# Kernel optimization log

Measured on AMD Instinct MI355X. Metric: run time of the kernel, lower is better.

Reference implementation:

```python
import jax, jax.numpy as jnp
import numpy as np

B, S, E, D, A = 32, 2048, 1024, 1024, 1024


def setup_inputs() -> dict:
    key = jax.random.key(0)
    k1, k2, k3, k4, k5, k6, k7, k8 = jax.random.split(key, 8)
    # Kaiming-uniform-ish init scales (values don't matter for correctness)
    def lin(kw, kb, fan_in, fan_out):
        bound = 1.0 / np.sqrt(fan_in)
        W = jax.random.uniform(kw, (fan_out, fan_in), minval=-bound, maxval=bound, dtype=jnp.float32)
        b = jax.random.uniform(kb, (fan_out,), minval=-bound, maxval=bound, dtype=jnp.float32)
        return W, b
    W_enc, b_enc = lin(k1, k2, E, A)
    W_dec, b_dec = lin(k3, k4, D, A)
    W_v, b_v = lin(k5, k6, A, 1)
    encoder_out = jax.random.normal(k7, (B, S, E), dtype=jnp.float32)
    decoder_hidden = jax.random.normal(k8, (B, D), dtype=jnp.float32)
    return {
        "encoder_out": encoder_out,
        "decoder_hidden": decoder_hidden,
        "W_enc": W_enc, "b_enc": b_enc,
        "W_dec": W_dec, "b_dec": b_dec,
        "W_v": W_v, "b_v": b_v,
    }


def reference(encoder_out, decoder_hidden, W_enc, b_enc, W_dec, b_dec, W_v, b_v):
    # encoder_proj: [B, S, A]
    encoder_proj = jnp.einsum('bse,ae->bsa', encoder_out, W_enc) + b_enc
    # decoder_proj: [B, 1, A]
    decoder_proj = (jnp.einsum('bd,ad->ba', decoder_hidden, W_dec) + b_dec)[:, None, :]
    # scores: [B, S] (V projects attention_dim -> 1)
    scores = jnp.einsum('bsa,a->bs', jnp.tanh(encoder_proj + decoder_proj), W_v[0]) + b_v[0]
    alpha = jax.nn.softmax(scores, axis=1)  # [B, S]
    context = jnp.einsum('bse,bs->be', encoder_out, alpha)  # [B, E]
    return (context, alpha)
```

## Files before the change

kernel.cpp:

```cpp
#include <hip/hip_runtime.h>

typedef unsigned short ushort_t;
typedef __attribute__((ext_vector_type(8))) short short8;
typedef __attribute__((ext_vector_type(4))) float f32x4;


__device__ __forceinline__ ushort_t f2bf(float f) {
    unsigned u = __builtin_bit_cast(unsigned, f);
    u += 0x7fffu + ((u >> 16) & 1u);
    return (ushort_t)(u >> 16);
}

__device__ __forceinline__ float bf2f(ushort_t h) {
    unsigned u = ((unsigned)h) << 16;
    return __builtin_bit_cast(float, u);
}

__device__ __forceinline__ float tanh_fast(float x) {
    float e = __expf(2.0f * x);
    float r = __builtin_amdgcn_rcpf(e + 1.0f);
    return __builtin_fmaf(-2.0f, r, 1.0f);
}

__device__ __forceinline__ void gld16(const ushort_t* g, ushort_t* lds) {
    __builtin_amdgcn_global_load_lds(
        (const __attribute__((address_space(1))) unsigned int*)g,
        (__attribute__((address_space(3))) unsigned int*)lds, 16, 0, 0);
}


__global__ __launch_bounds__(256) void k_front(const float* __restrict__ enc,
                                               const float* __restrict__ Wenc,
                                               const float* __restrict__ dh,
                                               const float* __restrict__ Wd,
                                               const float* __restrict__ bd,
                                               const float* __restrict__ be,
                                               ushort_t* __restrict__ encB,
                                               ushort_t* __restrict__ wencB,
                                               float* __restrict__ dproj,
                                               float4* __restrict__ scores4) {
    const int bx = blockIdx.x;
    const int t = threadIdx.x;
    if (bx < 8192) {
        int i = bx * 256 + t;
        for (; i < 17055744; i += 2097152) {
            if (i < 16777216) {
                float4 v = ((const float4*)enc)[i];
                ushort4 o;
                o.x = f2bf(v.x); o.y = f2bf(v.y); o.z = f2bf(v.z); o.w = f2bf(v.w);
                ((ushort4*)encB)[i] = o;
            } else if (i < 17039360) {
                int j = i - 16777216;
                float4 v = ((const float4*)Wenc)[j];
                ushort4 o;
                o.x = f2bf(v.x); o.y = f2bf(v.y); o.z = f2bf(v.z); o.w = f2bf(v.w);
                ((ushort4*)wencB)[j] = o;
            } else {
                scores4[i - 17039360] = (float4){0.f, 0.f, 0.f, 0.f};
            }
        }
    } else {
        int wid = (bx - 8192) * 4 + (t >> 6);
        int lane = t & 63;
        int a = wid & 1023, b = wid >> 10;
        const float4* x = (const float4*)(dh + (size_t)b * 1024);
        const float4* wrow = (const float4*)(Wd + (size_t)a * 1024);
        float s = 0.f;
#pragma unroll
        for (int it = 0; it < 4; ++it) {
            int c = it * 64 + lane;
            float4 xv = x[c], wv = wrow[c];
            s += xv.x * wv.x + xv.y * wv.y + xv.z * wv.z + xv.w * wv.w;
        }
#pragma unroll
        for (int o = 1; o < 64; o <<= 1) s += __shfl_xor(s, o, 64);
        if (lane == 0) dproj[b * 1024 + a] = s + bd[a] + be[a];
    }
}


__global__ __launch_bounds__(512, 2) void k_gemm_scores(const ushort_t* __restrict__ A,
                                                        const ushort_t* __restrict__ Bm,
                                                        const float* __restrict__ dproj,
                                                        const float* __restrict__ Wv,
                                                        float* __restrict__ scores) {
    __shared__ __align__(16) ushort_t At[2][256 * 64];
    __shared__ __align__(16) ushort_t Bt[2][256 * 64];

    const int tid = threadIdx.x;
    const int lane = tid & 63;
    const int w = tid >> 6;
    const int wm = w >> 2, wn = w & 3;

    const int blk = blockIdx.x;
    const int xcd = blk & 7;
    const int idx = blk >> 3;
    const int blkN = idx & 3;
    const int blkM = xcd + ((idx >> 2) << 3);
    const long long arow0 = (long long)blkM * 256;
    const int brow0 = blkN * 256;

    const int sr = lane >> 3;
    const int sgrp = lane & 7;
    const int c8s = sgrp ^ sr;

    const int q = lane >> 4;
    const int ml = lane & 15;

    const ushort_t* ga = A + (arow0 + w * 8 + sr) * 1024 + c8s * 8;
    const ushort_t* gb = Bm + (long long)(brow0 + w * 8 + sr) * 1024 + c8s * 8;

    f32x4 acc[8][4];
#pragma unroll
    for (int i = 0; i < 8; ++i)
#pragma unroll
        for (int jj = 0; jj < 4; ++jj) acc[i][jj] = (f32x4){0.f, 0.f, 0.f, 0.f};

#pragma unroll
    for (int j = 0; j < 4; ++j) gld16(ga + j * 65536, &At[0][w * 512 + j * 4096]);
#pragma unroll
    for (int j = 0; j < 4; ++j) gld16(gb + j * 65536, &Bt[0][w * 512 + j * 4096]);
    ga += 64; gb += 64;
    __builtin_amdgcn_s_waitcnt(0);
    __syncthreads();

    for (int t = 0; t < 16; ++t) {
        const int cur = t & 1;
        if (t < 15) {
            const int nxt = cur ^ 1;
#pragma unroll
            for (int j = 0; j < 4; ++j) gld16(ga + j * 65536, &At[nxt][w * 512 + j * 4096]);
#pragma unroll
            for (int j = 0; j < 4; ++j) gld16(gb + j * 65536, &Bt[nxt][w * 512 + j * 4096]);
            ga += 64; gb += 64;
        }
#pragma unroll
        for (int kk = 0; kk < 2; ++kk) {
            const int kb = kk * 4;
            const int slot = (kb + q) ^ (ml & 7);
            short8 af[8], bfr[4];
#pragma unroll
            for (int i = 0; i < 8; ++i) {
                int row = wm * 128 + i * 16 + ml;
                af[i] = *(const short8*)&At[cur][row * 64 + slot * 8];
            }
#pragma unroll
            for (int jj = 0; jj < 4; ++jj) {
                int col = wn * 64 + jj * 16 + ml;
                bfr[jj] = *(const short8*)&Bt[cur][col * 64 + slot * 8];
            }
            __builtin_amdgcn_s_setprio(1);
#pragma unroll
            for (int i = 0; i < 8; ++i)
#pragma unroll
                for (int jj = 0; jj < 4; ++jj)
                    acc[i][jj] = __builtin_amdgcn_mfma_f32_16x16x32_bf16(
                        af[i], bfr[jj], acc[i][jj], 0, 0, 0);
            __builtin_amdgcn_s_setprio(0);
        }
        __builtin_amdgcn_s_waitcnt(0);
        __syncthreads();
    }

    const int bb = blkM >> 3;
    float dp[4], wv[4];
#pragma unroll
    for (int jj = 0; jj < 4; ++jj) {
        int a = blkN * 256 + wn * 64 + jj * 16 + ml;
        dp[jj] = dproj[bb * 1024 + a];
        wv[jj] = Wv[a];
    }
#pragma unroll
    for (int i = 0; i < 8; ++i) {
        float rs[4] = {0.f, 0.f, 0.f, 0.f};
#pragma unroll
        for (int jj = 0; jj < 4; ++jj) {
            f32x4 v = acc[i][jj];
            rs[0] += wv[jj] * tanh_fast(v.x + dp[jj]);
            rs[1] += wv[jj] * tanh_fast(v.y + dp[jj]);
            rs[2] += wv[jj] * tanh_fast(v.z + dp[jj]);
            rs[3] += wv[jj] * tanh_fast(v.w + dp[jj]);
        }
#pragma unroll
        for (int r = 0; r < 4; ++r)
#pragma unroll
            for (int o = 1; o < 16; o <<= 1) rs[r] += __shfl_xor(rs[r], o, 64);
        if (ml == 0) {
            long long m0 = arow0 + wm * 128 + i * 16 + q * 4;
            atomicAdd(&scores[m0 + 0], rs[0]);
            atomicAdd(&scores[m0 + 1], rs[1]);
            atomicAdd(&scores[m0 + 2], rs[2]);
            atomicAdd(&scores[m0 + 3], rs[3]);
        }
    }
}


__global__ __launch_bounds__(512) void k_ctx(const ushort_t* __restrict__ encB,
                                             const float* __restrict__ scores,
                                             float* __restrict__ out) {
    const int b = blockIdx.x, ec = blockIdx.y;
    const int t = threadIdx.x;
    const int l = t & 31, g = t >> 5;
    const int lane = t & 63, wv = t >> 6;
    __shared__ float al[2048];
    __shared__ float red[8];
    __shared__ f32x4 part[16][33];

    float4 v = ((const float4*)scores)[b * 512 + t];
    float mx = fmaxf(fmaxf(v.x, v.y), fmaxf(v.z, v.w));
#pragma unroll
    for (int o = 1; o < 64; o <<= 1) mx = fmaxf(mx, __shfl_xor(mx, o, 64));
    if (lane == 0) red[wv] = mx;
    __syncthreads();
    mx = red[0];
#pragma unroll
    for (int j = 1; j < 8; ++j) mx = fmaxf(mx, red[j]);
    float e0 = __expf(v.x - mx), e1 = __expf(v.y - mx);
    float e2 = __expf(v.z - mx), e3 = __expf(v.w - mx);
    float s = e0 + e1 + e2 + e3;
#pragma unroll
    for (int o = 1; o < 64; o <<= 1) s += __shfl_xor(s, o, 64);
    __syncthreads();
    if (lane == 0) red[wv] = s;
    __syncthreads();
    s = 0.f;
#pragma unroll
    for (int j = 0; j < 8; ++j) s += red[j];
    float inv = 1.0f / s;
    float4 a4 = (float4){e0 * inv, e1 * inv, e2 * inv, e3 * inv};
    ((float4*)al)[t] = a4;
    if (ec == 0) ((float4*)(out + 32768 + (size_t)b * 2048))[t] = a4;
    __syncthreads();

    const ushort_t* ep = encB + ((size_t)b * 2048 + g) * 1024 + ec * 128 + l * 4;
    f32x4 acc = (f32x4){0.f, 0.f, 0.f, 0.f};
#pragma unroll 8
    for (int it = 0; it < 128; ++it) {
        ushort4 ev = *(const ushort4*)(ep + (size_t)it * 16384);
        float a = al[g + it * 16];
        acc.x += a * bf2f(ev.x);
        acc.y += a * bf2f(ev.y);
        acc.z += a * bf2f(ev.z);
        acc.w += a * bf2f(ev.w);
    }
    part[g][l] = acc;
    __syncthreads();
    if (t < 32) {
        f32x4 ss = part[0][t];
#pragma unroll
        for (int gg = 1; gg < 16; ++gg) {
            f32x4 pp = part[gg][t];
            ss.x += pp.x; ss.y += pp.y; ss.z += pp.z; ss.w += pp.w;
        }
        *(float4*)(out + (size_t)b * 1024 + ec * 128 + t * 4) =
            (float4){ss.x, ss.y, ss.z, ss.w};
    }
}


extern "C" void kernel_launch(void* const* d_in, const int* in_sizes, int n_in,
                              void* d_out, int out_size, void* d_ws, size_t ws_size,
                              hipStream_t stream) {
    const float* enc  = (const float*)d_in[0];
    const float* dh   = (const float*)d_in[1];
    const float* Wenc = (const float*)d_in[2];
    const float* benc = (const float*)d_in[3];
    const float* Wdec = (const float*)d_in[4];
    const float* bdec = (const float*)d_in[5];
    const float* Wv   = (const float*)d_in[6];
    float* out = (float*)d_out;

    char* ws = (char*)d_ws;
    ushort_t* encB  = (ushort_t*)ws;
    ushort_t* wencB = (ushort_t*)(ws + 134217728ull);
    float* dproj    = (float*)(ws + 134217728ull + 2097152ull);
    float* scores   = (float*)(ws + 134217728ull + 2097152ull + 131072ull);

    k_front<<<16384, 256, 0, stream>>>(enc, Wenc, dh, Wdec, bdec, benc,
                                       encB, wencB, dproj, (float4*)scores);
    k_gemm_scores<<<1024, 512, 0, stream>>>(encB, wencB, dproj, Wv, scores);
    k_ctx<<<dim3(32, 8), 512, 0, stream>>>(encB, scores, out);
}
```

Measured before the change: 574.1 us.

## Triple-buffer A tiles and use counted vmcnt waits in scores GEMM

The GEMM main loop moves from a double-buffered A/B pipeline with a full waitcnt(0) per step to a triple-buffered A and double-buffered B rotation. It uses explicit s_waitcnt vmcnt(N) so each iteration waits only for the tile it is about to consume, leaving later prefetches in flight. The intent is to hide more global-load latency behind MFMA work and stop draining the load queue every iteration. The cost is LDS use rising from 128KB to 160KB per block, which fills the CU's LDS. The hand-counted vmcnt values must exactly match the load issue order.

```diff
diff --git a/kernel.cpp b/kernel.cpp
--- a/kernel.cpp
+++ b/kernel.cpp
@@ -84,7 +84,7 @@
                                                         const float* __restrict__ dproj,
                                                         const float* __restrict__ Wv,
                                                         float* __restrict__ scores) {
-    __shared__ __align__(16) ushort_t At[2][256 * 64];
+    __shared__ __align__(16) ushort_t At[3][256 * 64];
     __shared__ __align__(16) ushort_t Bt[2][256 * 64];
 
     const int tid = threadIdx.x;
@@ -107,8 +107,8 @@
     const int q = lane >> 4;
     const int ml = lane & 15;
 
-    const ushort_t* ga = A + (arow0 + w * 8 + sr) * 1024 + c8s * 8;
-    const ushort_t* gb = Bm + (long long)(brow0 + w * 8 + sr) * 1024 + c8s * 8;
+    const ushort_t* gA = A + (arow0 + w * 8 + sr) * 1024 + c8s * 8;
+    const ushort_t* gB = Bm + (long long)(brow0 + w * 8 + sr) * 1024 + c8s * 8;
 
     f32x4 acc[8][4];
 #pragma unroll
@@ -116,24 +116,27 @@
 #pragma unroll
         for (int jj = 0; jj < 4; ++jj) acc[i][jj] = (f32x4){0.f, 0.f, 0.f, 0.f};
 
-#pragma unroll
-    for (int j = 0; j < 4; ++j) gld16(ga + j * 65536, &At[0][w * 512 + j * 4096]);
-#pragma unroll
-    for (int j = 0; j < 4; ++j) gld16(gb + j * 65536, &Bt[0][w * 512 + j * 4096]);
-    ga += 64; gb += 64;
-    __builtin_amdgcn_s_waitcnt(0);
-    __syncthreads();
+    ushort_t* a0 = At[0]; ushort_t* a1 = At[1]; ushort_t* a2 = At[2];
+    ushort_t* b0 = Bt[0]; ushort_t* b1 = Bt[1];
+
+    auto stage = [&](const ushort_t* src, ushort_t* dst) {
+#pragma unroll
+        for (int j = 0; j < 4; ++j) gld16(src + j * 65536, dst + w * 512 + j * 4096);
+    };
+
+    stage(gA, a0); gA += 64;
+    stage(gB, b0); gB += 64;
+    stage(gA, a1); gA += 64;
+    stage(gB, b1); gB += 64;
+    stage(gA, a2); gA += 64;
 
     for (int t = 0; t < 16; ++t) {
-        const int cur = t & 1;
-        if (t < 15) {
-            const int nxt = cur ^ 1;
-#pragma unroll
-            for (int j = 0; j < 4; ++j) gld16(ga + j * 65536, &At[nxt][w * 512 + j * 4096]);
-#pragma unroll
-            for (int j = 0; j < 4; ++j) gld16(gb + j * 65536, &Bt[nxt][w * 512 + j * 4096]);
-            ga += 64; gb += 64;
-        }
+        if (t < 14)       asm volatile("s_waitcnt vmcnt(12)" ::: "memory");
+        else if (t == 14) asm volatile("s_waitcnt vmcnt(8)"  ::: "memory");
+        else              asm volatile("s_waitcnt vmcnt(0)"  ::: "memory");
+        __builtin_amdgcn_s_barrier();
+        asm volatile("" ::: "memory");
+
 #pragma unroll
         for (int kk = 0; kk < 2; ++kk) {
             const int kb = kk * 4;
@@ -142,12 +145,12 @@
 #pragma unroll
             for (int i = 0; i < 8; ++i) {
                 int row = wm * 128 + i * 16 + ml;
-                af[i] = *(const short8*)&At[cur][row * 64 + slot * 8];
+                af[i] = *(const short8*)&a0[row * 64 + slot * 8];
             }
 #pragma unroll
             for (int jj = 0; jj < 4; ++jj) {
                 int col = wn * 64 + jj * 16 + ml;
-                bfr[jj] = *(const short8*)&Bt[cur][col * 64 + slot * 8];
+                bfr[jj] = *(const short8*)&b0[col * 64 + slot * 8];
             }
             __builtin_amdgcn_s_setprio(1);
 #pragma unroll
@@ -158,8 +161,16 @@
                         af[i], bfr[jj], acc[i][jj], 0, 0, 0);
             __builtin_amdgcn_s_setprio(0);
         }
-        __builtin_amdgcn_s_waitcnt(0);
-        __syncthreads();
+
+        asm volatile("" ::: "memory");
+        __builtin_amdgcn_s_barrier();
+        asm volatile("" ::: "memory");
+
+        if (t <= 13) { stage(gB, b0); gB += 64; }
+        if (t <= 12) { stage(gA, a0); gA += 64; }
+
+        ushort_t* tA = a0; a0 = a1; a1 = a2; a2 = tA;
+        ushort_t* tB = b0; b0 = b1; b1 = tB;
     }
 
     const int bb = blkM >> 3;
```

Result: no change. 566.2 us (-1.4%).
